# Performance work log

Measured on AMD Instinct MI355X. Metric: run time of the kernel, lower is better.

Reference implementation:

```python
import jax, jax.numpy as jnp
import numpy as np

N_EMBD = 1024
N_HEAD = 16
DIM_HEAD = N_EMBD // N_HEAD
SCALE = DIM_HEAD ** (-0.5)  # source divides by this (i.e. multiplies scores by sqrt(dim_head))


def setup_inputs() -> dict:
    key = jax.random.key(0)
    k1, k2, k3, k4, k5 = jax.random.split(key, 5)
    B, Tq, Tkv = 2, 2048, 2048
    x_q = jax.random.normal(k1, (B, Tq, N_EMBD), dtype=jnp.float32)
    x_kv = jax.random.normal(k2, (B, Tkv, N_EMBD), dtype=jnp.float32)
    s = 0.02
    W_q = jax.random.normal(k3, (N_EMBD, N_EMBD), dtype=jnp.float32) * s
    W_kv = jax.random.normal(k4, (N_EMBD, 2 * N_EMBD), dtype=jnp.float32) * s
    W_proj = jax.random.normal(k5, (N_EMBD, N_EMBD), dtype=jnp.float32) * s
    return {"x_q": x_q, "x_kv": x_kv, "W_q": W_q, "W_kv": W_kv, "W_proj": W_proj}


def reference(x_q, x_kv, W_q, W_kv, W_proj):
    B, Tq, C = x_q.shape
    Tkv = x_kv.shape[1]
    q = x_q @ W_q                      # [B, Tq, C]
    kv = x_kv @ W_kv                   # [B, Tkv, 2C]
    k, v = jnp.split(kv, 2, axis=2)
    # [B, H, T, Dh]
    q = q.reshape(B, Tq, N_HEAD, DIM_HEAD).transpose(0, 2, 1, 3)
    k = k.reshape(B, Tkv, N_HEAD, DIM_HEAD).transpose(0, 2, 1, 3)
    v = v.reshape(B, Tkv, N_HEAD, DIM_HEAD).transpose(0, 2, 1, 3)
    # Faithful to source: scores = q@k^T / scale  (== * sqrt(dim_head))
    attn = jnp.einsum('bhqd,bhkd->bhqk', q, k) / SCALE
    attn = jax.nn.softmax(attn, axis=-1)
    y = jnp.einsum('bhqk,bhkd->bhqd', attn, v)
    y = y.transpose(0, 2, 1, 3).reshape(B, Tq, C)
    return y @ W_proj
```

## Files before the change

kernel.cpp:

```cpp
#include <hip/hip_runtime.h>
#include <cstddef>

typedef _Float16 f16;
typedef _Float16 f16x8 __attribute__((ext_vector_type(8)));
typedef _Float16 f16x4 __attribute__((ext_vector_type(4)));
typedef _Float16 f16x2 __attribute__((ext_vector_type(2)));
typedef float f32x4 __attribute__((ext_vector_type(4)));
typedef float f32x16 __attribute__((ext_vector_type(16)));
typedef unsigned int u32;

__device__ inline float exp2_fast(float x) {
  float r;
  asm("v_exp_f32 %0, %1" : "=v"(r) : "v"(x));
  return r;
}

__device__ inline int pk2(float x, float y) {
  return __builtin_bit_cast(int, __builtin_amdgcn_cvt_pkrtz(x, y));
}

__device__ inline f16x2 pk2h(float x, float y) {
  return __builtin_bit_cast(f16x2, __builtin_amdgcn_cvt_pkrtz(x, y));
}

__device__ inline void permlane32_swap(int& a, int& b) {
  asm volatile("v_permlane32_swap_b32 %0, %1" : "+v"(a), "+v"(b));
}

__global__ __launch_bounds__(256) void prep(
    const float* __restrict__ xq, const float* __restrict__ xkv,
    f16* __restrict__ oq, f16* __restrict__ okv,
    const float* __restrict__ Wq, const float* __restrict__ Wkv,
    const float* __restrict__ Wp, f16* __restrict__ Wqt,
    f16* __restrict__ Wkvt, f16* __restrict__ Wpt) {
  __shared__ float t[32][33];
  int bid = blockIdx.x;
  if (bid < 8192) {
    const float* in = (bid < 4096) ? xq : xkv;
    f16* out = (bid < 4096) ? oq : okv;
    int i = ((bid & 4095) * 256 + threadIdx.x) * 4;
    float4 v = *(const float4*)&in[i];
    f16x4 h;
    h[0] = (f16)v.x; h[1] = (f16)v.y; h[2] = (f16)v.z; h[3] = (f16)v.w;
    *(f16x4*)&out[i] = h;
  } else {
    int zz = bid - 8192;
    int bx = zz & 31, by = (zz >> 5) & 31, z = zz >> 10;
    const float* in;
    f16* out;
    int N = 1024, extra = 0;
    if (z == 0) { in = Wq; out = Wqt; }
    else if (z == 3) { in = Wp; out = Wpt; }
    else { in = Wkv; out = Wkvt; N = 2048; extra = (z - 1) * 1024; }
    int tx = threadIdx.x % 32, ty = threadIdx.x / 32;
    int n0 = bx * 32 + extra, k0 = by * 32;
#pragma unroll
    for (int i = 0; i < 32; i += 8)
      t[ty + i][tx] = in[(size_t)(k0 + ty + i) * N + n0 + tx];
    __syncthreads();
#pragma unroll
    for (int i = 0; i < 32; i += 8)
      out[(size_t)(n0 + ty + i) * 1024 + k0 + tx] = (f16)t[tx][ty + i];
  }
}

template <int BN, typename CT>
__device__ __forceinline__ void gemm_body(
    const f16* __restrict__ A, const f16* __restrict__ Bt, CT* __restrict__ C,
    int bid, int M, int N, int K, float scale, f16* As, f16* Bs) {
  constexpr int NT = BN / 32;
  constexpr int BI = BN / 32;
  const int nb = N / BN;
  const int m0 = (bid / nb) * 128;
  const int n0 = (bid % nb) * BN;
  const int tid = threadIdx.x;
  const int w = tid >> 6, lane = tid & 63;
  const int l16 = lane & 15, quad = lane >> 4;
  const int wrow = (w >> 1) * 64, wcol = (w & 1) * (BN / 2);
  const int sr = tid >> 3, sc8 = tid & 7;
  const int wc8 = sc8 ^ (sr & 7);

  f32x4 acc[4][NT] = {};
  f16x8 ar[4], br[BI];

#pragma unroll
  for (int i = 0; i < 4; i++)
    ar[i] = *(const f16x8*)&A[(size_t)(m0 + sr + i * 32) * K + sc8 * 8];
#pragma unroll
  for (int i = 0; i < BI; i++)
    br[i] = *(const f16x8*)&Bt[(size_t)(n0 + sr + i * 32) * K + sc8 * 8];

  for (int k0 = 0; k0 < K; k0 += 64) {
#pragma unroll
    for (int i = 0; i < 4; i++)
      *(f16x8*)&As[(sr + i * 32) * 64 + wc8 * 8] = ar[i];
#pragma unroll
    for (int i = 0; i < BI; i++)
      *(f16x8*)&Bs[(sr + i * 32) * 64 + wc8 * 8] = br[i];
    __syncthreads();

    if (k0 + 64 < K) {
#pragma unroll
      for (int i = 0; i < 4; i++)
        ar[i] = *(const f16x8*)&A[(size_t)(m0 + sr + i * 32) * K + k0 + 64 + sc8 * 8];
#pragma unroll
      for (int i = 0; i < BI; i++)
        br[i] = *(const f16x8*)&Bt[(size_t)(n0 + sr + i * 32) * K + k0 + 64 + sc8 * 8];
    }

    f16x8 bf[NT][2];
#pragma unroll
    for (int nt = 0; nt < NT; nt++) {
      const int row = wcol + nt * 16 + l16;
#pragma unroll
      for (int s = 0; s < 2; s++)
        bf[nt][s] = *(const f16x8*)&Bs[row * 64 + (((s * 4 + quad) ^ (row & 7)) << 3)];
    }
#pragma unroll
    for (int mt = 0; mt < 4; mt++) {
      const int row = wrow + mt * 16 + l16;
      f16x8 af0 = *(const f16x8*)&As[row * 64 + ((quad ^ (row & 7)) << 3)];
      f16x8 af1 = *(const f16x8*)&As[row * 64 + (((4 + quad) ^ (row & 7)) << 3)];
#pragma unroll
      for (int nt = 0; nt < NT; nt++) {
        acc[mt][nt] = __builtin_amdgcn_mfma_f32_16x16x32_f16(af0, bf[nt][0], acc[mt][nt], 0, 0, 0);
        acc[mt][nt] = __builtin_amdgcn_mfma_f32_16x16x32_f16(af1, bf[nt][1], acc[mt][nt], 0, 0, 0);
      }
    }
    __syncthreads();
  }

#pragma unroll
  for (int mt = 0; mt < 4; mt++)
#pragma unroll
    for (int nt = 0; nt < NT; nt++)
#pragma unroll
      for (int r = 0; r < 4; r++) {
        int row = m0 + wrow + mt * 16 + quad * 4 + r;
        int col = n0 + wcol + nt * 16 + l16;
        C[(size_t)row * N + col] = (CT)(acc[mt][nt][r] * scale);
      }
}

__global__ __launch_bounds__(256, 3) void qkv_gemm(
    const f16* __restrict__ Xq, const f16* __restrict__ Wqt, f16* __restrict__ Qh,
    const f16* __restrict__ Xkv, const f16* __restrict__ Wkvt, f16* __restrict__ KVh,
    float sc_q) {
  __shared__ f16 As[128 * 64];
  __shared__ f16 Bs[128 * 64];
  if (blockIdx.x < 256)
    gemm_body<128, f16>(Xq, Wqt, Qh, blockIdx.x, 4096, 1024, 1024, sc_q, As, Bs);
  else
    gemm_body<128, f16>(Xkv, Wkvt, KVh, blockIdx.x - 256, 4096, 2048, 1024, 1.0f, As, Bs);
}

template <int BN, typename CT>
__global__ __launch_bounds__(256, 2) void gemm_lds(
    const f16* __restrict__ A, const f16* __restrict__ Bt, CT* __restrict__ C,
    int M, int N, int K, float scale) {
  __shared__ f16 As[128 * 64];
  __shared__ f16 Bs[BN * 64];
  gemm_body<BN, CT>(A, Bt, C, blockIdx.x, M, N, K, scale, As, Bs);
}

__global__ __launch_bounds__(512, 4) void attn_kernel(
    const f16* __restrict__ Qh, const f16* __restrict__ KVh, f16* __restrict__ Yh) {
  __shared__ f16 smem[18432];

  const int bid = blockIdx.x;
  const int hb = bid & 31;
  const int qt = bid >> 5;
  const int h = hb >> 1, b = hb & 1;
  const int tid = threadIdx.x;
  const int w = tid >> 6, lane = tid & 63;
  const int l31 = lane & 31, e = lane >> 5;
  const int qw = w & 3, half = w >> 2;
  const int tl = tid & 255;

  f16* Ks = smem + half * (2 * 64 * 72);
  f16* Vt = Ks + 64 * 72;

  const size_t qrow0 = (size_t)b * 2048 + (size_t)qt * 128;
  const size_t kvrow0 = (size_t)b * 2048 + (size_t)half * 1024;

  f16x8 qf[4];
#pragma unroll
  for (int ks = 0; ks < 4; ks++)
    qf[ks] = *(const f16x8*)&Qh[(qrow0 + qw * 32 + l31) * 1024 + h * 64 + ks * 16 + e * 8];

  float m_run = -1e30f, l_run = 0.0f;
  f32x16 o_acc[2] = {};

  const int ksr = tl >> 2, ksc = (tl & 3) << 4;
  const int vkv0 = (tl >> 3) * 2;
  const int vd0 = (tl & 7) * 8;
  const int vcol = ((((vkv0 >> 3) ^ (tl & 7)) << 3) | (vkv0 & 7));

  f16x8 kr0, kr1, vr0, vr1;
  {
    const f16* kb = &KVh[(kvrow0 + ksr) * 2048 + h * 64 + ksc];
    kr0 = *(const f16x8*)kb;
    kr1 = *(const f16x8*)(kb + 8);
    const f16* vb = &KVh[(kvrow0 + vkv0) * 2048 + 1024 + h * 64 + vd0];
    vr0 = *(const f16x8*)vb;
    vr1 = *(const f16x8*)(vb + 2048);
  }

  for (int t = 0; t < 16; t++) {
    *(f16x8*)&Ks[ksr * 72 + ksc] = kr0;
    *(f16x8*)&Ks[ksr * 72 + ksc + 8] = kr1;
#pragma unroll
    for (int j = 0; j < 8; j++) {
      f16x2 p; p[0] = vr0[j]; p[1] = vr1[j];
      *(f16x2*)&Vt[(vd0 + j) * 72 + vcol] = p;
    }
    __syncthreads();

    if (t + 1 < 16) {
      const f16* kb = &KVh[(kvrow0 + (t + 1) * 64 + ksr) * 2048 + h * 64 + ksc];
      kr0 = *(const f16x8*)kb;
      kr1 = *(const f16x8*)(kb + 8);
      const f16* vb = &KVh[(kvrow0 + (t + 1) * 64 + vkv0) * 2048 + 1024 + h * 64 + vd0];
      vr0 = *(const f16x8*)vb;
      vr1 = *(const f16x8*)(vb + 2048);
    }

    f32x16 sacc[2] = {};
#pragma unroll
    for (int kvt = 0; kvt < 2; kvt++)
#pragma unroll
      for (int ks = 0; ks < 4; ks++) {
        f16x8 a = *(const f16x8*)&Ks[(kvt * 32 + l31) * 72 + ks * 16 + e * 8];
        sacc[kvt] = __builtin_amdgcn_mfma_f32_32x32x16_f16(a, qf[ks], sacc[kvt], 0, 0, 0);
      }

    float mxa[4];
#pragma unroll
    for (int j = 0; j < 4; j++) {
      float a = fmaxf(fmaxf(sacc[0][j], sacc[0][j + 4]),
                      fmaxf(sacc[0][j + 8], sacc[0][j + 12]));
      float bb = fmaxf(fmaxf(sacc[1][j], sacc[1][j + 4]),
                       fmaxf(sacc[1][j + 8], sacc[1][j + 12]));
      mxa[j] = fmaxf(a, bb);
    }
    float mx = fmaxf(fmaxf(mxa[0], mxa[1]), fmaxf(mxa[2], mxa[3]));
    mx = fmaxf(mx, __shfl_xor(mx, 32, 64));

    if (!__all(mx <= m_run + 8.0f)) {
      float mnew = fmaxf(m_run, mx);
      float alpha = exp2_fast(m_run - mnew);
      m_run = mnew;
      l_run *= alpha;
#pragma unroll
      for (int r = 0; r < 16; r++) { o_acc[0][r] *= alpha; o_acc[1][r] *= alpha; }
    }

    float ss0 = 0.0f, ss1 = 0.0f, ss2 = 0.0f, ss3 = 0.0f;
#pragma unroll
    for (int kvt = 0; kvt < 2; kvt++)
#pragma unroll
      for (int r = 0; r < 16; r += 4) {
        float p0 = exp2_fast(sacc[kvt][r + 0] - m_run);
        float p1 = exp2_fast(sacc[kvt][r + 1] - m_run);
        float p2 = exp2_fast(sacc[kvt][r + 2] - m_run);
        float p3 = exp2_fast(sacc[kvt][r + 3] - m_run);
        sacc[kvt][r + 0] = p0; sacc[kvt][r + 1] = p1;
        sacc[kvt][r + 2] = p2; sacc[kvt][r + 3] = p3;
        ss0 += p0; ss1 += p1; ss2 += p2; ss3 += p3;
      }
    float ssum = (ss0 + ss1) + (ss2 + ss3);
    ssum += __shfl_xor(ssum, 32, 64);
    l_run += ssum;

    f16x8 pf[4];
#pragma unroll
    for (int kvt = 0; kvt < 2; kvt++)
#pragma unroll
      for (int hf = 0; hf < 2; hf++) {
        const int h8 = hf * 8;
        int a0 = pk2(sacc[kvt][h8 + 0], sacc[kvt][h8 + 1]);
        int b0 = pk2(sacc[kvt][h8 + 4], sacc[kvt][h8 + 5]);
        int a1 = pk2(sacc[kvt][h8 + 2], sacc[kvt][h8 + 3]);
        int b1 = pk2(sacc[kvt][h8 + 6], sacc[kvt][h8 + 7]);
        permlane32_swap(a0, b0);
        permlane32_swap(a1, b1);
        union { int i[4]; f16x8 v; } u;
        u.i[0] = a0; u.i[1] = a1; u.i[2] = b0; u.i[3] = b1;
        pf[kvt * 2 + hf] = u.v;
      }

#pragma unroll
    for (int dt = 0; dt < 2; dt++) {
      const int d = dt * 32 + l31;
      const int dx = d >> 3;
#pragma unroll
      for (int ks = 0; ks < 4; ks++) {
        f16x8 va = *(const f16x8*)&Vt[d * 72 + (((ks * 2 + e) ^ dx) << 3)];
        o_acc[dt] = __builtin_amdgcn_mfma_f32_32x32x16_f16(va, pf[ks], o_acc[dt], 0, 0, 0);
      }
    }
    __syncthreads();
  }

  float* Om = (float*)smem;
  float* ML = (float*)smem + 4 * 32 * 68;
  if (half == 1) {
#pragma unroll
    for (int dt = 0; dt < 2; dt++)
#pragma unroll
      for (int r2 = 0; r2 < 4; r2++) {
        f32x4 vv;
        vv[0] = o_acc[dt][r2 * 4 + 0];
        vv[1] = o_acc[dt][r2 * 4 + 1];
        vv[2] = o_acc[dt][r2 * 4 + 2];
        vv[3] = o_acc[dt][r2 * 4 + 3];
        *(f32x4*)&Om[(qw * 32 + l31) * 68 + dt * 32 + r2 * 8 + e * 4] = vv;
      }
    ML[qw * 64 + l31] = m_run;
    ML[qw * 64 + 32 + l31] = l_run;
  }
  __syncthreads();
  float linv = 0.0f;
  if (half == 0) {
    float m1 = ML[qw * 64 + l31], l1 = ML[qw * 64 + 32 + l31];
    float mm = fmaxf(m_run, m1);
    float a0 = exp2_fast(m_run - mm), a1 = exp2_fast(m1 - mm);
    linv = 1.0f / (l_run * a0 + l1 * a1);
#pragma unroll
    for (int dt = 0; dt < 2; dt++)
#pragma unroll
      for (int r2 = 0; r2 < 4; r2++) {
        f32x4 o1 = *(const f32x4*)&Om[(qw * 32 + l31) * 68 + dt * 32 + r2 * 8 + e * 4];
#pragma unroll
        for (int j = 0; j < 4; j++)
          o_acc[dt][r2 * 4 + j] = o_acc[dt][r2 * 4 + j] * a0 + o1[j] * a1;
      }
  }
  __syncthreads();

  if (half == 0) {
    f16* Of = smem + qw * 32 * 72;
#pragma unroll
    for (int dt = 0; dt < 2; dt++)
#pragma unroll
      for (int r2 = 0; r2 < 4; r2++) {
        f16x2 h0 = pk2h(o_acc[dt][r2 * 4 + 0] * linv, o_acc[dt][r2 * 4 + 1] * linv);
        f16x2 h1 = pk2h(o_acc[dt][r2 * 4 + 2] * linv, o_acc[dt][r2 * 4 + 3] * linv);
        f16x4 hh; hh[0] = h0[0]; hh[1] = h0[1]; hh[2] = h1[0]; hh[3] = h1[1];
        *(f16x4*)&Of[l31 * 72 + dt * 32 + r2 * 8 + e * 4] = hh;
      }
    const int qq = lane >> 1, dh = (lane & 1) * 32;
#pragma unroll
    for (int j = 0; j < 4; j++) {
      f16x8 v = *(const f16x8*)&Of[qq * 72 + dh + j * 8];
      *(f16x8*)&Yh[(qrow0 + qw * 32 + qq) * 1024 + h * 64 + dh + j * 8] = v;
    }
  }
}

extern "C" void kernel_launch(void* const* d_in, const int* in_sizes, int n_in,
                              void* d_out, int out_size, void* d_ws, size_t ws_size,
                              hipStream_t stream) {
  const float* x_q  = (const float*)d_in[0];
  const float* x_kv = (const float*)d_in[1];
  const float* W_q  = (const float*)d_in[2];
  const float* W_kv = (const float*)d_in[3];
  const float* W_p  = (const float*)d_in[4];
  float* out = (float*)d_out;

  f16* Wq_t  = (f16*)d_ws;
  f16* Wkv_t = Wq_t  + (size_t)1024 * 1024;
  f16* Wp_t  = Wkv_t + (size_t)2048 * 1024;
  f16* Qh    = Wp_t  + (size_t)1024 * 1024;
  f16* KVh   = Qh    + (size_t)4096 * 1024;
  f16* Yh    = KVh   + (size_t)4096 * 2048;
  f16* Xq_h  = Yh;
  f16* Xkv_h = Yh    + (size_t)4096 * 1024;

  prep<<<12288, 256, 0, stream>>>(x_q, x_kv, Xq_h, Xkv_h,
                                  W_q, W_kv, W_p, Wq_t, Wkv_t, Wp_t);

  const float SC = 11.5415603f;
  qkv_gemm<<<768, 256, 0, stream>>>(Xq_h, Wq_t, Qh, Xkv_h, Wkv_t, KVh, SC);

  attn_kernel<<<512, 512, 0, stream>>>(Qh, KVh, Yh);

  gemm_lds<64, float><<<512, 256, 0, stream>>>(Yh, Wp_t, out, 4096, 1024, 1024, 1.0f);
}
```

Baseline: 203.9 us.

## Use direct global-to-LDS loads in GEMM with XCD-aware block remap

```diff
diff --git a/kernel.cpp b/kernel.cpp
--- a/kernel.cpp
+++ b/kernel.cpp
@@ -25,6 +25,12 @@
 
 __device__ inline void permlane32_swap(int& a, int& b) {
   asm volatile("v_permlane32_swap_b32 %0, %1" : "+v"(a), "+v"(b));
+}
+
+__device__ __forceinline__ void gload16(const f16* g, f16* l) {
+  __builtin_amdgcn_global_load_lds(
+      (const __attribute__((address_space(1))) void*)g,
+      (__attribute__((address_space(3))) void*)l, 16, 0, 0);
 }
 
 __global__ __launch_bounds__(256) void prep(
@@ -69,44 +75,31 @@
     const f16* __restrict__ A, const f16* __restrict__ Bt, CT* __restrict__ C,
     int bid, int M, int N, int K, float scale, f16* As, f16* Bs) {
   constexpr int NT = BN / 32;
-  constexpr int BI = BN / 32;
   const int nb = N / BN;
-  const int m0 = (bid / nb) * 128;
-  const int n0 = (bid % nb) * BN;
+  const int nwg = (M / 128) * nb;
+  const int sbid = (bid & 7) * (nwg >> 3) + (bid >> 3);
+  const int m0 = (sbid / nb) * 128;
+  const int n0 = (sbid % nb) * BN;
   const int tid = threadIdx.x;
   const int w = tid >> 6, lane = tid & 63;
   const int l16 = lane & 15, quad = lane >> 4;
   const int wrow = (w >> 1) * 64, wcol = (w & 1) * (BN / 2);
-  const int sr = tid >> 3, sc8 = tid & 7;
-  const int wc8 = sc8 ^ (sr & 7);
+  const int lrow = lane >> 3, lcol = (lane & 7) * 8;
 
   f32x4 acc[4][NT] = {};
-  f16x8 ar[4], br[BI];
-
-#pragma unroll
-  for (int i = 0; i < 4; i++)
-    ar[i] = *(const f16x8*)&A[(size_t)(m0 + sr + i * 32) * K + sc8 * 8];
-#pragma unroll
-  for (int i = 0; i < BI; i++)
-    br[i] = *(const f16x8*)&Bt[(size_t)(n0 + sr + i * 32) * K + sc8 * 8];
 
   for (int k0 = 0; k0 < K; k0 += 64) {
 #pragma unroll
-    for (int i = 0; i < 4; i++)
-      *(f16x8*)&As[(sr + i * 32) * 64 + wc8 * 8] = ar[i];
-#pragma unroll
-    for (int i = 0; i < BI; i++)
-      *(f16x8*)&Bs[(sr + i * 32) * 64 + wc8 * 8] = br[i];
-    __syncthreads();
-
-    if (k0 + 64 < K) {
-#pragma unroll
-      for (int i = 0; i < 4; i++)
-        ar[i] = *(const f16x8*)&A[(size_t)(m0 + sr + i * 32) * K + k0 + 64 + sc8 * 8];
-#pragma unroll
-      for (int i = 0; i < BI; i++)
-        br[i] = *(const f16x8*)&Bt[(size_t)(n0 + sr + i * 32) * K + k0 + 64 + sc8 * 8];
-    }
+    for (int i = 0; i < 4; i++) {
+      const int r = w * 32 + i * 8;
+      gload16(&A[(size_t)(m0 + r + lrow) * K + k0 + lcol], &As[r * 64]);
+    }
+#pragma unroll
+    for (int i = 0; i < NT; i++) {
+      const int r = w * (BN / 4) + i * 8;
+      gload16(&Bt[(size_t)(n0 + r + lrow) * K + k0 + lcol], &Bs[r * 64]);
+    }
+    __syncthreads();
 
     f16x8 bf[NT][2];
 #pragma unroll
@@ -114,13 +107,13 @@
       const int row = wcol + nt * 16 + l16;
 #pragma unroll
       for (int s = 0; s < 2; s++)
-        bf[nt][s] = *(const f16x8*)&Bs[row * 64 + (((s * 4 + quad) ^ (row & 7)) << 3)];
+        bf[nt][s] = *(const f16x8*)&Bs[row * 64 + s * 32 + quad * 8];
     }
 #pragma unroll
     for (int mt = 0; mt < 4; mt++) {
       const int row = wrow + mt * 16 + l16;
-      f16x8 af0 = *(const f16x8*)&As[row * 64 + ((quad ^ (row & 7)) << 3)];
-      f16x8 af1 = *(const f16x8*)&As[row * 64 + (((4 + quad) ^ (row & 7)) << 3)];
+      f16x8 af0 = *(const f16x8*)&As[row * 64 + quad * 8];
+      f16x8 af1 = *(const f16x8*)&As[row * 64 + 32 + quad * 8];
 #pragma unroll
       for (int nt = 0; nt < NT; nt++) {
         acc[mt][nt] = __builtin_amdgcn_mfma_f32_16x16x32_f16(af0, bf[nt][0], acc[mt][nt], 0, 0, 0);
```

Result: no change. 203.5 us (-0.2%).
